# Optimization experiments

Measured on AMD Instinct MI355X. Metric: run time of the kernel, lower is better.

Reference implementation:

```python
import jax, jax.numpy as jnp
import numpy as np

VOCAB, EMB, WIN = 32000, 300, 5
H1, H2, NY, NZ = 300, 300, 128, 128
B, S = 32, 512


def setup_inputs() -> dict:
    key = jax.random.key(0)
    ks = jax.random.split(key, 16)
    sc = 0.05
    inp = {
        "x": jax.random.randint(ks[0], (B, S, WIN), 0, VOCAB),
        "emb": jax.random.normal(ks[1], (VOCAB, EMB), jnp.float32) * sc,
        "W_ih1": jax.random.normal(ks[2], (H1, EMB * WIN), jnp.float32) * sc,
        "W_hh1": jax.random.normal(ks[3], (H1, H1), jnp.float32) * sc,
        "b_ih1": jax.random.normal(ks[4], (H1,), jnp.float32) * sc,
        "b_hh1": jax.random.normal(ks[5], (H1,), jnp.float32) * sc,
        "W_ih2": jax.random.normal(ks[6], (H2, H1), jnp.float32) * sc,
        "W_hh2": jax.random.normal(ks[7], (H2, H2), jnp.float32) * sc,
        "b_ih2": jax.random.normal(ks[8], (H2,), jnp.float32) * sc,
        "b_hh2": jax.random.normal(ks[9], (H2,), jnp.float32) * sc,
        "fc1_w": jax.random.normal(ks[10], (NY, H1), jnp.float32) * sc,
        "fc1_b": jax.random.normal(ks[11], (NY,), jnp.float32) * sc,
        "fc2_w": jax.random.normal(ks[12], (NZ, H2), jnp.float32) * sc,
        "fc2_b": jax.random.normal(ks[13], (NZ,), jnp.float32) * sc,
    }
    return inp


def reference(x, emb, W_ih1, W_hh1, b_ih1, b_hh1, W_ih2, W_hh2, b_ih2, b_hh2,
              fc1_w, fc1_b, fc2_w, fc2_b):
    b, s, w = x.shape
    xe = emb[jnp.transpose(x, (1, 0, 2))].reshape(s, b, w * emb.shape[1])
    xe = jax.nn.relu(xe)

    h1_0 = jnp.zeros((b, W_hh1.shape[0]), xe.dtype)
    h2_0 = jnp.zeros((b, W_hh2.shape[0]), xe.dtype)

    def step(carry, xt):
        h1, h2 = carry
        h1 = jnp.tanh(xt @ W_ih1.T + b_ih1 + h1 @ W_hh1.T + b_hh1)
        h2 = jnp.tanh(h1 @ W_ih2.T + b_ih2 + h2 @ W_hh2.T + b_hh2)
        return (h1, h2), (h1, h2)

    _, (out1, out2) = jax.lax.scan(step, (h1_0, h2_0), xe)  # [S,B,H]

    out1 = jnp.transpose(out1, (1, 0, 2)).reshape(b * s, -1)
    out2 = jnp.transpose(out2, (1, 0, 2)).reshape(b * s, -1)
    out1 = out1 @ fc1_w.T + fc1_b
    out2 = out2 @ fc2_w.T + fc2_b
    return (out1, out2)
```

## Files before the change

kernel.cpp:

```cpp
#include <hip/hip_runtime.h>
#include <hip/hip_fp16.h>

#define S_LEN 512
#define BATCH 32
#define CHUNK 16

typedef _Float16 hv2  __attribute__((ext_vector_type(2)));
typedef _Float16 half8 __attribute__((ext_vector_type(8)));
typedef float    f32x4 __attribute__((ext_vector_type(4)));

__device__ __forceinline__ float dot2f(hv2 a, hv2 b, float c) {
#if __has_builtin(__builtin_amdgcn_fdot2)
    return __builtin_amdgcn_fdot2(a, b, c, false);
#else
    return c + (float)a.x * (float)b.x + (float)a.y * (float)b.y;
#endif
}

__device__ __forceinline__ float fast_tanh(float x) {
    float e = __expf(2.f * x);
    return 1.f - 2.f / (e + 1.f);
}

__device__ __forceinline__ void lds_barrier() {
    __asm__ volatile("s_waitcnt lgkmcnt(0)\n\ts_barrier" ::: "memory");
}
__device__ __forceinline__ void vm_drain() {
    __asm__ volatile("s_waitcnt vmcnt(0)" ::: "memory");
}

#define E8   1280000
#define W18  64000
#define W28  12800
#define FF8  5120
#define PREP_TOTAL8 (E8 + W18 + W28 + FF8 + FF8)

__global__ __launch_bounds__(256) void k_prep(
    const float* __restrict__ emb,  const float* __restrict__ Wih1,
    const float* __restrict__ Wih2, const float* __restrict__ fc1w,
    const float* __restrict__ fc2w,
    _Float16* __restrict__ embf, _Float16* __restrict__ Wf1,
    _Float16* __restrict__ Wf2,  _Float16* __restrict__ F1,
    _Float16* __restrict__ F2,   unsigned int* __restrict__ flags)
{
    int gid = blockIdx.x * 256 + threadIdx.x;
    if (gid < 64) flags[gid] = 0u;
    if (gid >= PREP_TOTAL8) return;

    half8 v;
    _Float16* dst;

    if (gid < E8) {
        int row = gid / 40, c8 = (gid - row * 40) * 8;
        #pragma unroll
        for (int j = 0; j < 8; ++j) {
            int c = c8 + j;
            float f = (c < 300) ? emb[(size_t)row * 300 + c] : 0.f;
            v[j] = (_Float16)(f > 0.f ? f : 0.f);
        }
        dst = embf + (size_t)gid * 8;
    } else if (gid < E8 + W18) {
        int i = gid - E8;
        int row = i / 200, c8 = (i - row * 200) * 8;
        #pragma unroll
        for (int j = 0; j < 8; ++j) {
            int c = c8 + j, w = c / 320, cc = c - w * 320;
            float f = (row < 300 && cc < 300) ? Wih1[(size_t)row * 1500 + w * 300 + cc] : 0.f;
            v[j] = (_Float16)f;
        }
        dst = Wf1 + (size_t)i * 8;
    } else if (gid < E8 + W18 + W28) {
        int i = gid - E8 - W18;
        int row = i / 40, c8 = (i - row * 40) * 8;
        #pragma unroll
        for (int j = 0; j < 8; ++j) {
            int c = c8 + j;
            float f = (row < 300 && c < 300) ? Wih2[(size_t)row * 300 + c] : 0.f;
            v[j] = (_Float16)f;
        }
        dst = Wf2 + (size_t)i * 8;
    } else if (gid < E8 + W18 + W28 + FF8) {
        int i = gid - E8 - W18 - W28;
        int row = i / 40, c8 = (i - row * 40) * 8;
        #pragma unroll
        for (int j = 0; j < 8; ++j) {
            int c = c8 + j;
            v[j] = (_Float16)((c < 300) ? fc1w[(size_t)row * 300 + c] : 0.f);
        }
        dst = F1 + (size_t)i * 8;
    } else {
        int i = gid - E8 - W18 - W28 - FF8;
        int row = i / 40, c8 = (i - row * 40) * 8;
        #pragma unroll
        for (int j = 0; j < 8; ++j) {
            int c = c8 + j;
            v[j] = (_Float16)((c < 300) ? fc2w[(size_t)row * 300 + c] : 0.f);
        }
        dst = F2 + (size_t)i * 8;
    }
    *(half8*)dst = v;
}

__global__ __launch_bounds__(256) void k_gemm1_mfma(
    const int* __restrict__ x, const _Float16* __restrict__ embf,
    const _Float16* __restrict__ Wf1, const float* __restrict__ b1,
    const float* __restrict__ b2, float* __restrict__ U)
{
    const int wid  = threadIdx.x >> 6;
    const int lane = threadIdx.x & 63;
    const int m    = lane & 15;
    const int q    = lane >> 4;
    const int r0   = blockIdx.x * 128 + wid * 32;
    const int n0   = blockIdx.y * 160;

    f32x4 acc[2][10];
    #pragma unroll
    for (int i = 0; i < 2; ++i)
        #pragma unroll
        for (int j = 0; j < 10; ++j)
            acc[i][j] = (f32x4){0.f, 0.f, 0.f, 0.f};

    const int rA = r0 + m, rB = r0 + 16 + m;
    const int xbA = ((rA & 31) * S_LEN + (rA >> 5)) * 5;
    const int xbB = ((rB & 31) * S_LEN + (rB >> 5)) * 5;

    for (int w = 0; w < 5; ++w) {
        const int idxA = x[xbA + w];
        const int idxB = x[xbB + w];
        const _Float16* ea = embf + (size_t)idxA * 320;
        const _Float16* eb = embf + (size_t)idxB * 320;
        const _Float16* wb = Wf1 + (size_t)w * 320;
        #pragma unroll
        for (int c = 0; c < 10; ++c) {
            const int k = c * 32 + q * 8;
            half8 a0 = *(const half8*)(ea + k);
            half8 a1 = *(const half8*)(eb + k);
            #pragma unroll
            for (int nt = 0; nt < 10; ++nt) {
                half8 bf = *(const half8*)(wb + (size_t)(n0 + nt * 16 + m) * 1600 + k);
                acc[0][nt] = __builtin_amdgcn_mfma_f32_16x16x32_f16(a0, bf, acc[0][nt], 0, 0, 0);
                acc[1][nt] = __builtin_amdgcn_mfma_f32_16x16x32_f16(a1, bf, acc[1][nt], 0, 0, 0);
            }
        }
    }

    #pragma unroll
    for (int nt = 0; nt < 10; ++nt) {
        const int n = n0 + nt * 16 + m;
        if (n >= 300) continue;
        const float bias = b1[n] + b2[n];
        #pragma unroll
        for (int mt = 0; mt < 2; ++mt) {
            const int rbase = r0 + mt * 16 + q * 4;
            #pragma unroll
            for (int reg = 0; reg < 4; ++reg)
                U[(size_t)(rbase + reg) * 300 + n] = acc[mt][nt][reg] + bias;
        }
    }
}

__global__ __launch_bounds__(256) void k_fc_mfma(
    const _Float16* __restrict__ H1, const _Float16* __restrict__ H2,
    const _Float16* __restrict__ F1, const _Float16* __restrict__ F2,
    const float* __restrict__ fb1, const float* __restrict__ fb2,
    float* __restrict__ out1, float* __restrict__ out2)
{
    const int layer = blockIdx.y;
    const _Float16* H = layer ? H2 : H1;
    const _Float16* F = layer ? F2 : F1;
    const float* bias = layer ? fb2 : fb1;
    float* out        = layer ? out2 : out1;

    const int wid  = threadIdx.x >> 6;
    const int lane = threadIdx.x & 63;
    const int m    = lane & 15;
    const int q    = lane >> 4;
    const int r0   = blockIdx.x * 128 + wid * 32;

    f32x4 acc[2][8];
    #pragma unroll
    for (int i = 0; i < 2; ++i)
        #pragma unroll
        for (int j = 0; j < 8; ++j)
            acc[i][j] = (f32x4){0.f, 0.f, 0.f, 0.f};

    const _Float16* ha = H + (size_t)(r0 + m) * 320;
    const _Float16* hb = H + (size_t)(r0 + 16 + m) * 320;

    #pragma unroll
    for (int c = 0; c < 10; ++c) {
        const int k = c * 32 + q * 8;
        half8 a0 = *(const half8*)(ha + k);
        half8 a1 = *(const half8*)(hb + k);
        #pragma unroll
        for (int nt = 0; nt < 8; ++nt) {
            half8 bf = *(const half8*)(F + (size_t)(nt * 16 + m) * 320 + k);
            acc[0][nt] = __builtin_amdgcn_mfma_f32_16x16x32_f16(a0, bf, acc[0][nt], 0, 0, 0);
            acc[1][nt] = __builtin_amdgcn_mfma_f32_16x16x32_f16(a1, bf, acc[1][nt], 0, 0, 0);
        }
    }

    #pragma unroll
    for (int nt = 0; nt < 8; ++nt) {
        const int n = nt * 16 + m;
        const float bv = bias[n];
        #pragma unroll
        for (int mt = 0; mt < 2; ++mt) {
            #pragma unroll
            for (int reg = 0; reg < 4; ++reg) {
                const int r = r0 + mt * 16 + q * 4 + reg;
                const int oidx = ((r & 31) * S_LEN + (r >> 5)) * 128 + n;
                out[oidx] = acc[mt][nt][reg] + bv;
            }
        }
    }
}

#define LDS_BYTES 52096

__device__ __forceinline__ void load_u_regs(float* up, const float* __restrict__ U1,
                                            int b, int t0) {
    #pragma unroll
    for (int j = 0; j < 10; ++j) {
        int e = threadIdx.x + 512 * j;
        int row = e / 300, col = e - row * 300;
        up[j] = (e < 4800) ? U1[((size_t)((t0 + row) * BATCH + b)) * 300 + col] : 0.f;
    }
}

__global__ __launch_bounds__(512) void k_rec_fused(
    const float* __restrict__ U1, const float* __restrict__ Whh1,
    const _Float16* __restrict__ Wf2, const float* __restrict__ Whh2,
    const float* __restrict__ bih2, const float* __restrict__ bhh2,
    _Float16* __restrict__ H1f, _Float16* __restrict__ H2f,
    unsigned int* __restrict__ flags)
{
    extern __shared__ char smem[];
    float   (*partials)[304] = (float(*)[304])smem;
    _Float16 (*hc)[320]      = (_Float16(*)[320])(smem + 12160);
    float   (*uc)[304]       = (float(*)[304])(smem + 22400);
    _Float16 (*h1s)[320]     = (_Float16(*)[320])(smem + 41856);

    const int tid  = threadIdx.x;
    const bool comp = tid < 500;
    const int g    = comp ? tid / 50 : 0;
    const int rt   = comp ? tid % 50 : 0;
    const int lane = tid & 63;
    const int wid  = tid >> 6;
    const int lm   = lane & 15;
    const int lq   = lane >> 4;

    for (int i = tid; i < CHUNK * 320; i += 512)
        ((_Float16*)hc)[i] = (_Float16)0.f;

    if (blockIdx.x < 32) {
        const int b = blockIdx.x;
        hv2 w1[6][16];
        if (comp) {
            #pragma unroll
            for (int i = 0; i < 6; ++i) {
                const float* wr = Whh1 + (size_t)(rt + 50 * i) * 300 + g * 32;
                #pragma unroll
                for (int j = 0; j < 16; ++j) {
                    int c0 = g * 32 + 2 * j;
                    hv2 p;
                    p.x = (c0     < 300) ? (_Float16)wr[2 * j]     : (_Float16)0.f;
                    p.y = (c0 + 1 < 300) ? (_Float16)wr[2 * j + 1] : (_Float16)0.f;
                    w1[i][j] = p;
                }
            }
        }

        float upref[10];
        load_u_regs(upref, U1, b, 0);

        for (int c = 0; c < 32; ++c) {
            const int t0 = c * CHUNK;
            if (c > 0) {
                const int tb = t0 - CHUNK;
                for (int i = tid; i < CHUNK * 40; i += 512) {
                    int row = i / 40, c8 = i - row * 40;
                    half8 v = *(const half8*)&hc[row][c8 * 8];
                    *(half8*)&H1f[((size_t)((tb + row) * BATCH + b)) * 320 + c8 * 8] = v;
                }
            }
            #pragma unroll
            for (int j = 0; j < 10; ++j) {
                int e = tid + 512 * j;
                if (e < 4800) {
                    int row = e / 300, col = e - row * 300;
                    uc[row][col] = upref[j];
                }
            }
            if (c > 0) {
                vm_drain();
                if (tid == 0)
                    __hip_atomic_store(&flags[b], (unsigned)t0,
                                       __ATOMIC_RELEASE, __HIP_MEMORY_SCOPE_AGENT);
            }
            if (c + 1 < 32)
                load_u_regs(upref, U1, b, t0 + CHUNK);
            lds_barrier();

            for (int s = 0; s < CHUNK; ++s) {
                if (comp) {
                    const half8* hp = (const half8*)&hc[(s - 1) & 15][g * 32];
                    float a0 = 0.f, a1 = 0.f, a2 = 0.f, a3 = 0.f, a4 = 0.f, a5 = 0.f;
                    #pragma unroll
                    for (int jj = 0; jj < 4; ++jj) {
                        half8 q8 = hp[jj];
                        const hv2* qv = (const hv2*)&q8;
                        #pragma unroll
                        for (int j4 = 0; j4 < 4; ++j4) {
                            const int j = 4 * jj + j4;
                            a0 = dot2f(w1[0][j], qv[j4], a0);
                            a1 = dot2f(w1[1][j], qv[j4], a1);
                            a2 = dot2f(w1[2][j], qv[j4], a2);
                            a3 = dot2f(w1[3][j], qv[j4], a3);
                            a4 = dot2f(w1[4][j], qv[j4], a4);
                            a5 = dot2f(w1[5][j], qv[j4], a5);
                        }
                    }
                    partials[g][rt]       = a0;
                    partials[g][rt + 50]  = a1;
                    partials[g][rt + 100] = a2;
                    partials[g][rt + 150] = a3;
                    partials[g][rt + 200] = a4;
                    partials[g][rt + 250] = a5;
                }
                lds_barrier();
                if (tid < 300) {
                    float ssum = uc[s][tid];
                    #pragma unroll
                    for (int g2 = 0; g2 < 10; ++g2)
                        ssum += partials[g2][tid];
                    hc[s][tid] = (_Float16)fast_tanh(ssum);
                }
                lds_barrier();
            }
        }
        {
            const int tb = S_LEN - CHUNK;
            for (int i = tid; i < CHUNK * 40; i += 512) {
                int row = i / 40, c8 = i - row * 40;
                half8 v = *(const half8*)&hc[row][c8 * 8];
                *(half8*)&H1f[((size_t)((tb + row) * BATCH + b)) * 320 + c8 * 8] = v;
            }
            vm_drain();
            if (tid == 0)
                __hip_atomic_store(&flags[b], (unsigned)S_LEN,
                                   __ATOMIC_RELEASE, __HIP_MEMORY_SCOPE_AGENT);
        }
    } else {
        const int b = blockIdx.x - 32;
        hv2 whh[6][16];
        if (comp) {
            #pragma unroll
            for (int i = 0; i < 6; ++i) {
                const float* wr = Whh2 + (size_t)(rt + 50 * i) * 300 + g * 32;
                #pragma unroll
                for (int j = 0; j < 16; ++j) {
                    int c0 = g * 32 + 2 * j;
                    hv2 p;
                    p.x = (c0     < 300) ? (_Float16)wr[2 * j]     : (_Float16)0.f;
                    p.y = (c0 + 1 < 300) ? (_Float16)wr[2 * j + 1] : (_Float16)0.f;
                    whh[i][j] = p;
                }
            }
        }
        float bias = (tid < 300) ? (bih2[tid] + bhh2[tid]) : 0.f;

        for (int c = 0; c < 32; ++c) {
            const int t0 = c * CHUNK;
            if (c > 0) {
                const int tb = t0 - CHUNK;
                for (int i = tid; i < CHUNK * 40; i += 512) {
                    int row = i / 40, c8 = i - row * 40;
                    half8 v = *(const half8*)&hc[row][c8 * 8];
                    *(half8*)&H2f[((size_t)((tb + row) * BATCH + b)) * 320 + c8 * 8] = v;
                }
            }
            if (tid == 0) {
                while (__hip_atomic_load(&flags[b], __ATOMIC_ACQUIRE,
                                         __HIP_MEMORY_SCOPE_AGENT) < (unsigned)(t0 + CHUNK))
                    __builtin_amdgcn_s_sleep(2);
            }
            __syncthreads();

            for (int i = tid; i < CHUNK * 40; i += 512) {
                int row = i / 40, c8 = i - row * 40;
                *(half8*)&h1s[row][c8 * 8] =
                    *(const half8*)&H1f[((size_t)((t0 + row) * BATCH + b)) * 320 + c8 * 8];
            }
            lds_barrier();

            for (int nt = wid; nt < 19; nt += 8) {
                f32x4 acc = (f32x4){0.f, 0.f, 0.f, 0.f};
                const int n = nt * 16 + lm;
                const _Float16* wrow = Wf2 + (size_t)n * 320;
                #pragma unroll
                for (int k0 = 0; k0 < 320; k0 += 32) {
                    half8 a  = *(const half8*)&h1s[lm][k0 + lq * 8];
                    half8 bf = *(const half8*)&wrow[k0 + lq * 8];
                    acc = __builtin_amdgcn_mfma_f32_16x16x32_f16(a, bf, acc, 0, 0, 0);
                }
                #pragma unroll
                for (int reg = 0; reg < 4; ++reg)
                    uc[lq * 4 + reg][n] = acc[reg];
            }
            lds_barrier();

            for (int s = 0; s < CHUNK; ++s) {
                if (comp) {
                    const half8* hp = (const half8*)&hc[(s - 1) & 15][g * 32];
                    float a0 = 0.f, a1 = 0.f, a2 = 0.f, a3 = 0.f, a4 = 0.f, a5 = 0.f;
                    #pragma unroll
                    for (int jj = 0; jj < 4; ++jj) {
                        half8 q8 = hp[jj];
                        const hv2* qv = (const hv2*)&q8;
                        #pragma unroll
                        for (int j4 = 0; j4 < 4; ++j4) {
                            const int j = 4 * jj + j4;
                            a0 = dot2f(whh[0][j], qv[j4], a0);
                            a1 = dot2f(whh[1][j], qv[j4], a1);
                            a2 = dot2f(whh[2][j], qv[j4], a2);
                            a3 = dot2f(whh[3][j], qv[j4], a3);
                            a4 = dot2f(whh[4][j], qv[j4], a4);
                            a5 = dot2f(whh[5][j], qv[j4], a5);
                        }
                    }
                    partials[g][rt]       = a0;
                    partials[g][rt + 50]  = a1;
                    partials[g][rt + 100] = a2;
                    partials[g][rt + 150] = a3;
                    partials[g][rt + 200] = a4;
                    partials[g][rt + 250] = a5;
                }
                lds_barrier();
                if (tid < 300) {
                    float ssum = bias + uc[s][tid];
                    #pragma unroll
                    for (int g2 = 0; g2 < 10; ++g2)
                        ssum += partials[g2][tid];
                    hc[s][tid] = (_Float16)fast_tanh(ssum);
                }
                lds_barrier();
            }
        }
        {
            const int tb = S_LEN - CHUNK;
            for (int i = tid; i < CHUNK * 40; i += 512) {
                int row = i / 40, c8 = i - row * 40;
                half8 v = *(const half8*)&hc[row][c8 * 8];
                *(half8*)&H2f[((size_t)((tb + row) * BATCH + b)) * 320 + c8 * 8] = v;
            }
        }
    }
}

extern "C" void kernel_launch(void* const* d_in, const int* in_sizes, int n_in,
                              void* d_out, int out_size, void* d_ws, size_t ws_size,
                              hipStream_t stream) {
    const int*   x     = (const int*)d_in[0];
    const float* emb   = (const float*)d_in[1];
    const float* Wih1  = (const float*)d_in[2];
    const float* Whh1  = (const float*)d_in[3];
    const float* bih1  = (const float*)d_in[4];
    const float* bhh1  = (const float*)d_in[5];
    const float* Wih2  = (const float*)d_in[6];
    const float* Whh2  = (const float*)d_in[7];
    const float* bih2  = (const float*)d_in[8];
    const float* bhh2  = (const float*)d_in[9];
    const float* fc1w  = (const float*)d_in[10];
    const float* fc1b  = (const float*)d_in[11];
    const float* fc2w  = (const float*)d_in[12];
    const float* fc2b  = (const float*)d_in[13];

    float* out1 = (float*)d_out;
    float* out2 = out1 + (size_t)16384 * 128;

    char* w = (char*)d_ws;
    float*        U1    = (float*)w;
    _Float16*     H1    = (_Float16*)(w + 19660800);
    _Float16*     Wf1   = (_Float16*)(w + 30146560);
    _Float16*     Wf2   = (_Float16*)(w + 31170560);
    _Float16*     F1    = (_Float16*)(w + 31375360);
    _Float16*     F2    = (_Float16*)(w + 31457280);
    unsigned int* flags = (unsigned int*)(w + 31539200);
    _Float16*     EMBF  = (_Float16*)(w + 31539456);
    _Float16*     H2    = EMBF;

    const int prep_blocks = (PREP_TOTAL8 + 255) / 256;
    k_prep<<<prep_blocks, 256, 0, stream>>>(emb, Wih1, Wih2, fc1w, fc2w,
                                            EMBF, Wf1, Wf2, F1, F2, flags);

    dim3 g(128, 2);
    k_gemm1_mfma<<<g, 256, 0, stream>>>(x, EMBF, Wf1, bih1, bhh1, U1);
    k_rec_fused<<<64, 512, LDS_BYTES, stream>>>(U1, Whh1, Wf2, Whh2, bih2, bhh2,
                                                H1, H2, flags);
    k_fc_mfma<<<g, 256, 0, stream>>>(H1, H2, F1, F2, fc1b, fc2b, out1, out2);
}
```

Measured before the change: 846.3 us.

## Split each recurrent row across thread pairs and reduce with shuffles, not LDS

The per-timestep recurrent matvec is reorganised. Each hidden row is now owned by two adjacent threads, each holding half of that row's weights in registers (76 packed half2 values). The two halves are combined with a lane shuffle instead of LDS partial sums, which removes one block barrier and the partials buffer from every serial step. The block grows to 640 threads, the bias add for layer 2 moves into the MFMA input projection, and the staging loops become single-pass. The cost is higher per-thread register pressure and more dot-product work per thread on the serial critical path.

Measured after the change: 914.7 us. 1.08x slower.

```diff
diff --git a/kernel.cpp b/kernel.cpp
--- a/kernel.cpp
+++ b/kernel.cpp
@@ -216,19 +216,19 @@
     }
 }
 
-#define LDS_BYTES 52096
+#define LDS_BYTES 39936
 
 __device__ __forceinline__ void load_u_regs(float* up, const float* __restrict__ U1,
                                             int b, int t0) {
     #pragma unroll
-    for (int j = 0; j < 10; ++j) {
-        int e = threadIdx.x + 512 * j;
+    for (int j = 0; j < 8; ++j) {
+        int e = threadIdx.x + 640 * j;
         int row = e / 300, col = e - row * 300;
         up[j] = (e < 4800) ? U1[((size_t)((t0 + row) * BATCH + b)) * 300 + col] : 0.f;
     }
 }
 
-__global__ __launch_bounds__(512) void k_rec_fused(
+__global__ __launch_bounds__(640, 2) void k_rec_fused(
     const float* __restrict__ U1, const float* __restrict__ Whh1,
     const _Float16* __restrict__ Wf2, const float* __restrict__ Whh2,
     const float* __restrict__ bih2, const float* __restrict__ bhh2,
@@ -236,60 +236,57 @@
     unsigned int* __restrict__ flags)
 {
     extern __shared__ char smem[];
-    float   (*partials)[304] = (float(*)[304])smem;
-    _Float16 (*hc)[320]      = (_Float16(*)[320])(smem + 12160);
-    float   (*uc)[304]       = (float(*)[304])(smem + 22400);
-    _Float16 (*h1s)[320]     = (_Float16(*)[320])(smem + 41856);
+    _Float16 (*hc)[320]  = (_Float16(*)[320])smem;
+    float    (*uc)[304]  = (float(*)[304])(smem + 10240);
+    _Float16 (*h1s)[320] = (_Float16(*)[320])(smem + 29696);
 
     const int tid  = threadIdx.x;
-    const bool comp = tid < 500;
-    const int g    = comp ? tid / 50 : 0;
-    const int rt   = comp ? tid % 50 : 0;
+    const int row  = tid >> 1;
+    const int half = tid & 1;
     const int lane = tid & 63;
     const int wid  = tid >> 6;
     const int lm   = lane & 15;
     const int lq   = lane >> 4;
 
-    for (int i = tid; i < CHUNK * 320; i += 512)
+    for (int i = tid; i < CHUNK * 320; i += 640)
         ((_Float16*)hc)[i] = (_Float16)0.f;
+
+    const bool act = row < 300;
+    const float* wsrc = (blockIdx.x < 32) ? Whh1 : Whh2;
+    hv2 w[76];
+    {
+        const float* wr = wsrc + (size_t)(act ? row : 0) * 300 + half * 152;
+        #pragma unroll
+        for (int j = 0; j < 76; ++j) {
+            int c0 = half * 152 + 2 * j;
+            hv2 p;
+            p.x = (act && c0     < 300) ? (_Float16)wr[2 * j]     : (_Float16)0.f;
+            p.y = (act && c0 + 1 < 300) ? (_Float16)wr[2 * j + 1] : (_Float16)0.f;
+            w[j] = p;
+        }
+    }
 
     if (blockIdx.x < 32) {
         const int b = blockIdx.x;
-        hv2 w1[6][16];
-        if (comp) {
-            #pragma unroll
-            for (int i = 0; i < 6; ++i) {
-                const float* wr = Whh1 + (size_t)(rt + 50 * i) * 300 + g * 32;
-                #pragma unroll
-                for (int j = 0; j < 16; ++j) {
-                    int c0 = g * 32 + 2 * j;
-                    hv2 p;
-                    p.x = (c0     < 300) ? (_Float16)wr[2 * j]     : (_Float16)0.f;
-                    p.y = (c0 + 1 < 300) ? (_Float16)wr[2 * j + 1] : (_Float16)0.f;
-                    w1[i][j] = p;
-                }
-            }
-        }
-
-        float upref[10];
+        float upref[8];
         load_u_regs(upref, U1, b, 0);
 
         for (int c = 0; c < 32; ++c) {
             const int t0 = c * CHUNK;
             if (c > 0) {
                 const int tb = t0 - CHUNK;
-                for (int i = tid; i < CHUNK * 40; i += 512) {
-                    int row = i / 40, c8 = i - row * 40;
-                    half8 v = *(const half8*)&hc[row][c8 * 8];
-                    *(half8*)&H1f[((size_t)((tb + row) * BATCH + b)) * 320 + c8 * 8] = v;
+                {
+                    int r16 = tid / 40, c8 = tid - r16 * 40;
+                    half8 v = *(const half8*)&hc[r16][c8 * 8];
+                    *(half8*)&H1f[((size_t)((tb + r16) * BATCH + b)) * 320 + c8 * 8] = v;
                 }
             }
             #pragma unroll
-            for (int j = 0; j < 10; ++j) {
-                int e = tid + 512 * j;
+            for (int j = 0; j < 8; ++j) {
+                int e = tid + 640 * j;
                 if (e < 4800) {
-                    int row = e / 300, col = e - row * 300;
-                    uc[row][col] = upref[j];
+                    int r = e / 300, col = e - r * 300;
+                    uc[r][col] = upref[j];
                 }
             }
             if (c > 0) {
@@ -303,49 +300,30 @@
             lds_barrier();
 
             for (int s = 0; s < CHUNK; ++s) {
-                if (comp) {
-                    const half8* hp = (const half8*)&hc[(s - 1) & 15][g * 32];
-                    float a0 = 0.f, a1 = 0.f, a2 = 0.f, a3 = 0.f, a4 = 0.f, a5 = 0.f;
-                    #pragma unroll
-                    for (int jj = 0; jj < 4; ++jj) {
-                        half8 q8 = hp[jj];
-                        const hv2* qv = (const hv2*)&q8;
-                        #pragma unroll
-                        for (int j4 = 0; j4 < 4; ++j4) {
-                            const int j = 4 * jj + j4;
-                            a0 = dot2f(w1[0][j], qv[j4], a0);
-                            a1 = dot2f(w1[1][j], qv[j4], a1);
-                            a2 = dot2f(w1[2][j], qv[j4], a2);
-                            a3 = dot2f(w1[3][j], qv[j4], a3);
-                            a4 = dot2f(w1[4][j], qv[j4], a4);
-                            a5 = dot2f(w1[5][j], qv[j4], a5);
-                        }
-                    }
-                    partials[g][rt]       = a0;
-                    partials[g][rt + 50]  = a1;
-                    partials[g][rt + 100] = a2;
-                    partials[g][rt + 150] = a3;
-                    partials[g][rt + 200] = a4;
-                    partials[g][rt + 250] = a5;
+                float uval = (row < 304) ? uc[s][row] : 0.f;
+                const half8* hp = (const half8*)&hc[(s - 1) & 15][half * 152];
+                float a0 = 0.f, a1 = 0.f, a2 = 0.f, a3 = 0.f;
+                #pragma unroll
+                for (int jj = 0; jj < 19; ++jj) {
+                    half8 q8 = hp[jj];
+                    const hv2* qv = (const hv2*)&q8;
+                    a0 = dot2f(w[4 * jj],     qv[0], a0);
+                    a1 = dot2f(w[4 * jj + 1], qv[1], a1);
+                    a2 = dot2f(w[4 * jj + 2], qv[2], a2);
+                    a3 = dot2f(w[4 * jj + 3], qv[3], a3);
                 }
-                lds_barrier();
-                if (tid < 300) {
-                    float ssum = uc[s][tid];
-                    #pragma unroll
-                    for (int g2 = 0; g2 < 10; ++g2)
-                        ssum += partials[g2][tid];
-                    hc[s][tid] = (_Float16)fast_tanh(ssum);
-                }
+                float acc = (a0 + a1) + (a2 + a3);
+                acc += __shfl_xor(acc, 1);
+                if (half == 0 && act)
+                    hc[s][row] = (_Float16)fast_tanh(acc + uval);
                 lds_barrier();
             }
         }
         {
             const int tb = S_LEN - CHUNK;
-            for (int i = tid; i < CHUNK * 40; i += 512) {
-                int row = i / 40, c8 = i - row * 40;
-                half8 v = *(const half8*)&hc[row][c8 * 8];
-                *(half8*)&H1f[((size_t)((tb + row) * BATCH + b)) * 320 + c8 * 8] = v;
-            }
+            int r16 = tid / 40, c8 = tid - r16 * 40;
+            half8 v = *(const half8*)&hc[r16][c8 * 8];
+            *(half8*)&H1f[((size_t)((tb + r16) * BATCH + b)) * 320 + c8 * 8] = v;
             vm_drain();
             if (tid == 0)
                 __hip_atomic_store(&flags[b], (unsigned)S_LEN,
@@ -353,32 +331,22 @@
         }
     } else {
         const int b = blockIdx.x - 32;
-        hv2 whh[6][16];
-        if (comp) {
-            #pragma unroll
-            for (int i = 0; i < 6; ++i) {
-                const float* wr = Whh2 + (size_t)(rt + 50 * i) * 300 + g * 32;
-                #pragma unroll
-                for (int j = 0; j < 16; ++j) {
-                    int c0 = g * 32 + 2 * j;
-                    hv2 p;
-                    p.x = (c0     < 300) ? (_Float16)wr[2 * j]     : (_Float16)0.f;
-                    p.y = (c0 + 1 < 300) ? (_Float16)wr[2 * j + 1] : (_Float16)0.f;
-                    whh[i][j] = p;
-                }
-            }
-        }
-        float bias = (tid < 300) ? (bih2[tid] + bhh2[tid]) : 0.f;
+
+        float bv0 = 0.f, bv1 = 0.f;
+        {
+            int n0 = wid * 16 + lm;
+            if (n0 < 300) bv0 = bih2[n0] + bhh2[n0];
+            int n1 = (wid + 10) * 16 + lm;
+            if (wid + 10 < 19 && n1 < 300) bv1 = bih2[n1] + bhh2[n1];
+        }
 
         for (int c = 0; c < 32; ++c) {
             const int t0 = c * CHUNK;
             if (c > 0) {
                 const int tb = t0 - CHUNK;
-                for (int i = tid; i < CHUNK * 40; i += 512) {
-                    int row = i / 40, c8 = i - row * 40;
-                    half8 v = *(const half8*)&hc[row][c8 * 8];
-                    *(half8*)&H2f[((size_t)((tb + row) * BATCH + b)) * 320 + c8 * 8] = v;
-                }
+                int r16 = tid / 40, c8 = tid - r16 * 40;
+                half8 v = *(const half8*)&hc[r16][c8 * 8];
+                *(half8*)&H2f[((size_t)((tb + r16) * BATCH + b)) * 320 + c8 * 8] = v;
             }
             if (tid == 0) {
                 while (__hip_atomic_load(&flags[b], __ATOMIC_ACQUIRE,
@@ -387,73 +355,59 @@
             }
             __syncthreads();
 
-            for (int i = tid; i < CHUNK * 40; i += 512) {
-                int row = i / 40, c8 = i - row * 40;
-                *(half8*)&h1s[row][c8 * 8] =
-                    *(const half8*)&H1f[((size_t)((t0 + row) * BATCH + b)) * 320 + c8 * 8];
+            {
+                int r16 = tid / 40, c8 = tid - r16 * 40;
+                *(half8*)&h1s[r16][c8 * 8] =
+                    *(const half8*)&H1f[((size_t)((t0 + r16) * BATCH + b)) * 320 + c8 * 8];
             }
             lds_barrier();
 
-            for (int nt = wid; nt < 19; nt += 8) {
-                f32x4 acc = (f32x4){0.f, 0.f, 0.f, 0.f};
-                const int n = nt * 16 + lm;
-                const _Float16* wrow = Wf2 + (size_t)n * 320;
+            #pragma unroll
+            for (int rep = 0; rep < 2; ++rep) {
+                const int nt = wid + rep * 10;
+                if (nt < 19) {
+                    f32x4 acc = (f32x4){0.f, 0.f, 0.f, 0.f};
+                    const int n = nt * 16 + lm;
+                    const _Float16* wrow = Wf2 + (size_t)n * 320;
+                    #pragma unroll
+                    for (int k0 = 0; k0 < 320; k0 += 32) {
+                        half8 a  = *(const half8*)&h1s[lm][k0 + lq * 8];
+                        half8 bf = *(const half8*)&wrow[k0 + lq * 8];
+                        acc = __builtin_amdgcn_mfma_f32_16x16x32_f16(a, bf, acc, 0, 0, 0);
+                    }
+                    const float bb = rep ? bv1 : bv0;
+                    #pragma unroll
+                    for (int reg = 0; reg < 4; ++reg)
+                        uc[lq * 4 + reg][n] = acc[reg] + bb;
+                }
+            }
+            lds_barrier();
+
+            for (int s = 0; s < CHUNK; ++s) {
+                float uval = (row < 304) ? uc[s][row] : 0.f;
+                const half8* hp = (const half8*)&hc[(s - 1) & 15][half * 152];
+                float a0 = 0.f, a1 = 0.f, a2 = 0.f, a3 = 0.f;
                 #pragma unroll
-                for (int k0 = 0; k0 < 320; k0 += 32) {
-                    half8 a  = *(const half8*)&h1s[lm][k0 + lq * 8];
-                    half8 bf = *(const half8*)&wrow[k0 + lq * 8];
-                    acc = __builtin_amdgcn_mfma_f32_16x16x32_f16(a, bf, acc, 0, 0, 0);
+                for (int jj = 0; jj < 19; ++jj) {
+                    half8 q8 = hp[jj];
+                    const hv2* qv = (const hv2*)&q8;
+                    a0 = dot2f(w[4 * jj],     qv[0], a0);
+                    a1 = dot2f(w[4 * jj + 1], qv[1], a1);
+                    a2 = dot2f(w[4 * jj + 2], qv[2], a2);
+                    a3 = dot2f(w[4 * jj + 3], qv[3], a3);
                 }
-                #pragma unroll
-                for (int reg = 0; reg < 4; ++reg)
-                    uc[lq * 4 + reg][n] = acc[reg];
-            }
-            lds_barrier();
-
-            for (int s = 0; s < CHUNK; ++s) {
-                if (comp) {
-                    const half8* hp = (const half8*)&hc[(s - 1) & 15][g * 32];
-                    float a0 = 0.f, a1 = 0.f, a2 = 0.f, a3 = 0.f, a4 = 0.f, a5 = 0.f;
-                    #pragma unroll
-                    for (int jj = 0; jj < 4; ++jj) {
-                        half8 q8 = hp[jj];
-                        const hv2* qv = (const hv2*)&q8;
-                        #pragma unroll
-                        for (int j4 = 0; j4 < 4; ++j4) {
-                            const int j = 4 * jj + j4;
-                            a0 = dot2f(whh[0][j], qv[j4], a0);
-                            a1 = dot2f(whh[1][j], qv[j4], a1);
-                            a2 = dot2f(whh[2][j], qv[j4], a2);
-                            a3 = dot2f(whh[3][j], qv[j4], a3);
-                            a4 = dot2f(whh[4][j], qv[j4], a4);
-                            a5 = dot2f(whh[5][j], qv[j4], a5);
-                        }
-                    }
-                    partials[g][rt]       = a0;
-                    partials[g][rt + 50]  = a1;
-                    partials[g][rt + 100] = a2;
-                    partials[g][rt + 150] = a3;
-                    partials[g][rt + 200] = a4;
-                    partials[g][rt + 250] = a5;
-                }
-                lds_barrier();
-                if (tid < 300) {
-                    float ssum = bias + uc[s][tid];
-                    #pragma unroll
-                    for (int g2 = 0; g2 < 10; ++g2)
-                        ssum += partials[g2][tid];
-                    hc[s][tid] = (_Float16)fast_tanh(ssum);
-                }
+                float acc = (a0 + a1) + (a2 + a3);
+                acc += __shfl_xor(acc, 1);
+                if (half == 0 && act)
+                    hc[s][row] = (_Float16)fast_tanh(acc + uval);
                 lds_barrier();
             }
         }
         {
             const int tb = S_LEN - CHUNK;
-            for (int i = tid; i < CHUNK * 40; i += 512) {
-                int row = i / 40, c8 = i - row * 40;
-                half8 v = *(const half8*)&hc[row][c8 * 8];
-                *(half8*)&H2f[((size_t)((tb + row) * BATCH + b)) * 320 + c8 * 8] = v;
-            }
+            int r16 = tid / 40, c8 = tid - r16 * 40;
+            half8 v = *(const half8*)&hc[r16][c8 * 8];
+            *(half8*)&H2f[((size_t)((tb + r16) * BATCH + b)) * 320 + c8 * 8] = v;
         }
     }
 }
@@ -496,7 +450,7 @@
 
     dim3 g(128, 2);
     k_gemm1_mfma<<<g, 256, 0, stream>>>(x, EMBF, Wf1, bih1, bhh1, U1);
-    k_rec_fused<<<64, 512, LDS_BYTES, stream>>>(U1, Whh1, Wf2, Whh2, bih2, bhh2,
+    k_rec_fused<<<64, 640, LDS_BYTES, stream>>>(U1, Whh1, Wf2, Whh2, bih2, bhh2,
                                                 H1, H2, flags);
     k_fc_mfma<<<g, 256, 0, stream>>>(H1, H2, F1, F2, fc1b, fc2b, out1, out2);
 }
```
